# Kernel optimization log

Measured on AMD Instinct MI355X. Metric: run time of the kernel, lower is better.

The kernel has to match this reference:

```python
import jax, jax.numpy as jnp
import numpy as np

N_NODES = 100000
N_EDGES = 2000000


def setup_inputs() -> dict:
    key = jax.random.key(0)
    ks = jax.random.split(key, 8)
    x = jax.random.normal(ks[0], (N_NODES, 8), dtype=jnp.float32)
    edge_index = jax.random.randint(ks[1], (2, N_EDGES), 0, N_NODES, dtype=jnp.int64)
    W1 = jax.random.normal(ks[2], (8, 32), dtype=jnp.float32) * (1.0 / np.sqrt(8))
    b1 = jnp.zeros((32,), dtype=jnp.float32)
    W2 = jax.random.normal(ks[3], (32, 32), dtype=jnp.float32) * (1.0 / np.sqrt(32))
    b2 = jnp.zeros((32,), dtype=jnp.float32)
    Wf = jax.random.normal(ks[4], (32, 1), dtype=jnp.float32) * (1.0 / np.sqrt(32))
    bf = jnp.zeros((1,), dtype=jnp.float32)
    return {"x": x, "edge_index": edge_index, "W1": W1, "b1": b1,
            "W2": W2, "b2": b2, "Wf": Wf, "bf": bf}


def _gcn_conv(x, src, dst, norm, W, b, n_nodes):
    # x: [N, Fin] -> [N, Fout]; standard PyG GCNConv with self-loops + sym norm
    h = x @ W                                   # [N, Fout]
    msg = h[src] * norm[:, None]                # gather + scale, [E+N, Fout]
    out = jax.ops.segment_sum(msg, dst, num_segments=n_nodes)  # scatter-add
    return out + b


def reference(x, edge_index, W1, b1, W2, b2, Wf, bf):
    n = x.shape[0]
    loop = jnp.arange(n, dtype=edge_index.dtype)
    src = jnp.concatenate([edge_index[0], loop])
    dst = jnp.concatenate([edge_index[1], loop])
    # symmetric normalization: deg from target indices (incl. self-loops)
    deg = jax.ops.segment_sum(jnp.ones_like(dst, dtype=x.dtype), dst, num_segments=n)
    dis = jnp.where(deg > 0, jax.lax.rsqrt(jnp.maximum(deg, 1e-12)), 0.0)
    norm = dis[src] * dis[dst]                  # [E+N]

    h = jax.nn.relu(_gcn_conv(x, src, dst, norm, W1, b1, n))
    h = jax.nn.relu(_gcn_conv(h, src, dst, norm, W2, b2, n))
    return h @ Wf + bf                          # [N, 1]
```

## Files before the change

### kernel.cpp

```cpp
#include <hip/hip_runtime.h>
#include <hip/hip_fp16.h>


#define NBLK 256
#define SHIFT 8
#define BMASK 255
#define NBUCK 512

__global__ void k_hist(const int* __restrict__ dst, int* __restrict__ part, int E) {
    __shared__ int hist[NBUCK];
    int t = threadIdx.x;
    hist[t] = 0; hist[t + 256] = 0;
    __syncthreads();
    int E4 = E >> 2;
    int chunk4 = (E4 + NBLK - 1) / NBLK;
    int b = blockIdx.x;
    int s4 = b * chunk4;
    int e4 = min(s4 + chunk4, E4);
    const int4* dst4 = (const int4*)dst;
    for (int i = s4 + t; i < e4; i += 256) {
        int4 d = dst4[i];
        atomicAdd(&hist[d.x >> SHIFT], 1);
        atomicAdd(&hist[d.y >> SHIFT], 1);
        atomicAdd(&hist[d.z >> SHIFT], 1);
        atomicAdd(&hist[d.w >> SHIFT], 1);
    }
    if (b == NBLK - 1) {
        for (int e = (E4 << 2) + t; e < E; e += 256)
            atomicAdd(&hist[dst[e] >> SHIFT], 1);
    }
    __syncthreads();
    part[(size_t)t * NBLK + b] = hist[t];
    part[(size_t)(t + 256) * NBLK + b] = hist[t + 256];
}

__global__ void k_scanA(int* __restrict__ part, int* __restrict__ btot) {
    int t = threadIdx.x;
    int b = blockIdx.x * 4 + (t >> 6);
    int lane = t & 63;
    int4* p4 = (int4*)(part + (size_t)b * NBLK);
    int4 v = p4[lane];
    int ls = v.x + v.y + v.z + v.w;
    int s = ls;
#pragma unroll
    for (int off = 1; off < 64; off <<= 1) {
        int u = __shfl_up(s, off, 64);
        if (lane >= off) s += u;
    }
    int base = s - ls;
    int4 o;
    o.x = base;
    o.y = base + v.x;
    o.z = o.y + v.y;
    o.w = o.z + v.z;
    p4[lane] = o;
    if (lane == 63) btot[b] = s;
}

__global__ void k_scanB(const int* __restrict__ btot, int* __restrict__ bbase,
                        int* __restrict__ rowptr, int n, int E) {
    __shared__ int tmp[NBUCK];
    int t = threadIdx.x;
    int v = btot[t];
    tmp[t] = v;
    __syncthreads();
    for (int off = 1; off < NBUCK; off <<= 1) {
        int add = (t >= off) ? tmp[t - off] : 0;
        __syncthreads();
        tmp[t] += add;
        __syncthreads();
    }
    bbase[t] = tmp[t] - v;
    if (t == NBUCK - 1) bbase[NBUCK] = tmp[NBUCK - 1];
    if (t == 0) rowptr[n] = E;
}

__global__ void k_binA2(const int* __restrict__ src, const int* __restrict__ dst,
                        const int* __restrict__ part, const int* __restrict__ bbase,
                        int* __restrict__ bpair, int E) {
    __shared__ int cur[NBUCK];
    int t = threadIdx.x;
    int b = blockIdx.x;
    cur[t] = part[(size_t)t * NBLK + b] + bbase[t];
    __syncthreads();
    int E4 = E >> 2;
    int chunk4 = (E4 + NBLK - 1) / NBLK;
    int s4 = b * chunk4;
    int e4 = min(s4 + chunk4, E4);
    const int4* src4 = (const int4*)src;
    const int4* dst4 = (const int4*)dst;
    for (int i = s4 + t; i < e4; i += 512) {
        int4 s = src4[i];
        int4 d = dst4[i];
        int p0 = atomicAdd(&cur[d.x >> SHIFT], 1);
        bpair[p0] = (s.x << SHIFT) | (d.x & BMASK);
        int p1 = atomicAdd(&cur[d.y >> SHIFT], 1);
        bpair[p1] = (s.y << SHIFT) | (d.y & BMASK);
        int p2 = atomicAdd(&cur[d.z >> SHIFT], 1);
        bpair[p2] = (s.z << SHIFT) | (d.z & BMASK);
        int p3 = atomicAdd(&cur[d.w >> SHIFT], 1);
        bpair[p3] = (s.w << SHIFT) | (d.w & BMASK);
    }
    if (b == NBLK - 1) {
        for (int e = (E4 << 2) + t; e < E; e += 512) {
            int sv = src[e], dv = dst[e];
            int p = atomicAdd(&cur[dv >> SHIFT], 1);
            bpair[p] = (sv << SHIFT) | (dv & BMASK);
        }
    }
}

__global__ void k_fill2(const int* __restrict__ bpair, const int* __restrict__ bbase,
                        const float* __restrict__ x,
                        int* __restrict__ rowptr, float* __restrict__ dis,
                        unsigned int* __restrict__ xs16, int* __restrict__ col, int n) {
    __shared__ int cnt[256];
    __shared__ int tmp[256];
    __shared__ int cur[256];
    __shared__ float sdis[256];
    int b = blockIdx.x;
    int t = threadIdx.x;
    int start = bbase[b], end = bbase[b + 1];
    if (t < 256) cnt[t] = 0;
    __syncthreads();
    for (int i = start + t; i < end; i += 512)
        atomicAdd(&cnt[bpair[i] & BMASK], 1);
    __syncthreads();
    int v0 = (t < 256) ? cnt[t] : 0;
    if (t < 256) tmp[t] = v0;
    __syncthreads();
    for (int off = 1; off < 256; off <<= 1) {
        int add = (t < 256 && t >= off) ? tmp[t - off] : 0;
        __syncthreads();
        if (t < 256) tmp[t] += add;
        __syncthreads();
    }
    if (t < 256) {
        int v = (b << SHIFT) + t;
        if (v < n) {
            int r = start + tmp[t] - v0;
            rowptr[v] = r;
            cur[t] = r;
            float dv = rsqrtf(1.0f + (float)v0);
            dis[v] = dv;
            sdis[t] = dv;
        }
    }
    __syncthreads();
    int ubase = (b << SHIFT) * 4;
    int nu = n * 4;
    const float2* x2 = (const float2*)x;
    for (int i = t; i < 1024; i += 512) {
        int gi = ubase + i;
        if (gi < nu) {
            float d = sdis[i >> 2];
            float2 xv = x2[gi];
            __half2 h2 = __float22half2_rn(make_float2(xv.x * d, xv.y * d));
            xs16[gi] = *(unsigned int*)&h2;
        }
    }
    for (int i = start + t; i < end; i += 512) {
        int p = bpair[i];
        int pos = atomicAdd(&cur[p & BMASK], 1);
        col[pos] = p >> SHIFT;
    }
}

__global__ void k_g1b(const int* __restrict__ rowptr, const int* __restrict__ col,
                      const uint4* __restrict__ xs16u4, const float* __restrict__ dis,
                      const float* __restrict__ W1, const float* __restrict__ b1,
                      const float* __restrict__ W2, uint2* __restrict__ g16u2, int n) {
    __shared__ float sW1[256];
    __shared__ float sW2[1024];
    __shared__ float sh[4][8][36];
    int t = threadIdx.x;
    sW1[t] = W1[t];
    for (int i = t; i < 1024; i += 256) sW2[i] = W2[i];
    __syncthreads();
    int widx = t >> 6, lane = t & 63;
    int nd = lane >> 3, j = lane & 7;
    int v = (blockIdx.x * 4 + widx) * 8 + nd;
    float a0 = 0.f, a1 = 0.f, a2 = 0.f, a3 = 0.f,
          a4 = 0.f, a5 = 0.f, a6 = 0.f, a7 = 0.f;
    int r0 = 0, r1 = 0;
    if (v < n) { r0 = rowptr[v]; r1 = rowptr[v + 1]; }
    for (int i = r0 + j; i < r1; i += 8) {
        uint4 raw = xs16u4[col[i]];
        float2 f0 = __half22float2(*(const __half2*)&raw.x);
        float2 f1 = __half22float2(*(const __half2*)&raw.y);
        float2 f2 = __half22float2(*(const __half2*)&raw.z);
        float2 f3 = __half22float2(*(const __half2*)&raw.w);
        a0 += f0.x; a1 += f0.y; a2 += f1.x; a3 += f1.y;
        a4 += f2.x; a5 += f2.y; a6 += f3.x; a7 += f3.y;
    }
    if (j == 0 && v < n) {
        uint4 raw = xs16u4[v];
        float2 f0 = __half22float2(*(const __half2*)&raw.x);
        float2 f1 = __half22float2(*(const __half2*)&raw.y);
        float2 f2 = __half22float2(*(const __half2*)&raw.z);
        float2 f3 = __half22float2(*(const __half2*)&raw.w);
        a0 += f0.x; a1 += f0.y; a2 += f1.x; a3 += f1.y;
        a4 += f2.x; a5 += f2.y; a6 += f3.x; a7 += f3.y;
    }
#pragma unroll
    for (int m = 1; m < 8; m <<= 1) {
        a0 += __shfl_xor(a0, m, 64);
        a1 += __shfl_xor(a1, m, 64);
        a2 += __shfl_xor(a2, m, 64);
        a3 += __shfl_xor(a3, m, 64);
        a4 += __shfl_xor(a4, m, 64);
        a5 += __shfl_xor(a5, m, 64);
        a6 += __shfl_xor(a6, m, 64);
        a7 += __shfl_xor(a7, m, 64);
    }
    float dv = (v < n) ? dis[v] : 0.f;
    int f0i = j * 4;
    float h0 = 0.f, h1 = 0.f, h2 = 0.f, h3 = 0.f;
    {
        float ak[8] = {a0, a1, a2, a3, a4, a5, a6, a7};
#pragma unroll
        for (int k = 0; k < 8; ++k) {
            float4 w = *(const float4*)&sW1[k * 32 + f0i];
            h0 += ak[k] * w.x; h1 += ak[k] * w.y;
            h2 += ak[k] * w.z; h3 += ak[k] * w.w;
        }
    }
    h0 = fmaxf(dv * h0 + b1[f0i + 0], 0.f);
    h1 = fmaxf(dv * h1 + b1[f0i + 1], 0.f);
    h2 = fmaxf(dv * h2 + b1[f0i + 2], 0.f);
    h3 = fmaxf(dv * h3 + b1[f0i + 3], 0.f);
    *(float4*)&sh[widx][nd][f0i] = make_float4(h0, h1, h2, h3);
    const float4* hrow = (const float4*)&sh[widx][nd][0];
    float4 hr[8];
#pragma unroll
    for (int k4 = 0; k4 < 8; ++k4) hr[k4] = hrow[k4];
    float g0 = 0.f, g1 = 0.f, g2 = 0.f, g3 = 0.f;
#pragma unroll
    for (int k4 = 0; k4 < 8; ++k4) {
        float hk[4] = {hr[k4].x, hr[k4].y, hr[k4].z, hr[k4].w};
#pragma unroll
        for (int m = 0; m < 4; ++m) {
            float4 w = *(const float4*)&sW2[(k4 * 4 + m) * 32 + f0i];
            g0 += hk[m] * w.x; g1 += hk[m] * w.y;
            g2 += hk[m] * w.z; g3 += hk[m] * w.w;
        }
    }
    if (v < n) {
        __half2 ha = __float22half2_rn(make_float2(g0 * dv, g1 * dv));
        __half2 hb = __float22half2_rn(make_float2(g2 * dv, g3 * dv));
        uint2 o;
        o.x = *(unsigned int*)&ha;
        o.y = *(unsigned int*)&hb;
        g16u2[(size_t)v * 8 + j] = o;
    }
}

__global__ void k_g2f(const int* __restrict__ rowptr, const int* __restrict__ col,
                      const uint4* __restrict__ g16u4, const float* __restrict__ dis,
                      const float* __restrict__ b2, const float* __restrict__ Wf,
                      const float* __restrict__ bf, float* __restrict__ out, int n) {
    int t = threadIdx.x;
    int wave = t >> 6, lane = t & 63;
    int nd = lane >> 3, sub = lane & 7;
    int slot = sub >> 2, q = sub & 3;
    int v = (blockIdx.x * 4 + wave) * 8 + nd;
    if (v >= n) return;
    int r0 = rowptr[v], r1 = rowptr[v + 1];
    float4 s0 = make_float4(0.f, 0.f, 0.f, 0.f);
    float4 s1 = make_float4(0.f, 0.f, 0.f, 0.f);
    float4 t0 = make_float4(0.f, 0.f, 0.f, 0.f);
    float4 t1 = make_float4(0.f, 0.f, 0.f, 0.f);
    if (slot == 0) {
        uint4 raw = g16u4[(size_t)v * 4 + q];
        float2 f0 = __half22float2(*(const __half2*)&raw.x);
        float2 f1 = __half22float2(*(const __half2*)&raw.y);
        float2 f2 = __half22float2(*(const __half2*)&raw.z);
        float2 f3 = __half22float2(*(const __half2*)&raw.w);
        s0.x += f0.x; s0.y += f0.y; s0.z += f1.x; s0.w += f1.y;
        s1.x += f2.x; s1.y += f2.y; s1.z += f3.x; s1.w += f3.y;
    }
    int i = r0 + slot;
    for (; i + 2 < r1; i += 4) {
        int cA = col[i], cB = col[i + 2];
        uint4 rawA = g16u4[(size_t)cA * 4 + q];
        uint4 rawB = g16u4[(size_t)cB * 4 + q];
        float2 a0 = __half22float2(*(const __half2*)&rawA.x);
        float2 a1 = __half22float2(*(const __half2*)&rawA.y);
        float2 a2 = __half22float2(*(const __half2*)&rawA.z);
        float2 a3 = __half22float2(*(const __half2*)&rawA.w);
        s0.x += a0.x; s0.y += a0.y; s0.z += a1.x; s0.w += a1.y;
        s1.x += a2.x; s1.y += a2.y; s1.z += a3.x; s1.w += a3.y;
        float2 b0 = __half22float2(*(const __half2*)&rawB.x);
        float2 b1v = __half22float2(*(const __half2*)&rawB.y);
        float2 b2v = __half22float2(*(const __half2*)&rawB.z);
        float2 b3 = __half22float2(*(const __half2*)&rawB.w);
        t0.x += b0.x; t0.y += b0.y; t0.z += b1v.x; t0.w += b1v.y;
        t1.x += b2v.x; t1.y += b2v.y; t1.z += b3.x; t1.w += b3.y;
    }
    if (i < r1) {
        uint4 raw = g16u4[(size_t)col[i] * 4 + q];
        float2 f0 = __half22float2(*(const __half2*)&raw.x);
        float2 f1 = __half22float2(*(const __half2*)&raw.y);
        float2 f2 = __half22float2(*(const __half2*)&raw.z);
        float2 f3 = __half22float2(*(const __half2*)&raw.w);
        s0.x += f0.x; s0.y += f0.y; s0.z += f1.x; s0.w += f1.y;
        s1.x += f2.x; s1.y += f2.y; s1.z += f3.x; s1.w += f3.y;
    }
    s0.x += t0.x; s0.y += t0.y; s0.z += t0.z; s0.w += t0.w;
    s1.x += t1.x; s1.y += t1.y; s1.z += t1.z; s1.w += t1.w;
    s0.x += __shfl_xor(s0.x, 4, 64);
    s0.y += __shfl_xor(s0.y, 4, 64);
    s0.z += __shfl_xor(s0.z, 4, 64);
    s0.w += __shfl_xor(s0.w, 4, 64);
    s1.x += __shfl_xor(s1.x, 4, 64);
    s1.y += __shfl_xor(s1.y, 4, 64);
    s1.z += __shfl_xor(s1.z, 4, 64);
    s1.w += __shfl_xor(s1.w, 4, 64);
    float dv = dis[v];
    float4 bv0 = ((const float4*)b2)[q * 2], bv1 = ((const float4*)b2)[q * 2 + 1];
    float4 wv0 = ((const float4*)Wf)[q * 2], wv1 = ((const float4*)Wf)[q * 2 + 1];
    float p = fmaxf(dv * s0.x + bv0.x, 0.f) * wv0.x
            + fmaxf(dv * s0.y + bv0.y, 0.f) * wv0.y
            + fmaxf(dv * s0.z + bv0.z, 0.f) * wv0.z
            + fmaxf(dv * s0.w + bv0.w, 0.f) * wv0.w
            + fmaxf(dv * s1.x + bv1.x, 0.f) * wv1.x
            + fmaxf(dv * s1.y + bv1.y, 0.f) * wv1.y
            + fmaxf(dv * s1.z + bv1.z, 0.f) * wv1.z
            + fmaxf(dv * s1.w + bv1.w, 0.f) * wv1.w;
    p += __shfl_xor(p, 1, 64);
    p += __shfl_xor(p, 2, 64);
    if (sub == 0) out[v] = p + bf[0];
}

extern "C" void kernel_launch(void* const* d_in, const int* in_sizes, int n_in,
                              void* d_out, int out_size, void* d_ws, size_t ws_size,
                              hipStream_t stream) {
    const float* x  = (const float*)d_in[0];
    const int*   ei = (const int*)d_in[1];
    const float* W1 = (const float*)d_in[2];
    const float* b1 = (const float*)d_in[3];
    const float* W2 = (const float*)d_in[4];
    const float* b2 = (const float*)d_in[5];
    const float* Wf = (const float*)d_in[6];
    const float* bf = (const float*)d_in[7];
    float* out = (float*)d_out;

    const int n = in_sizes[0] / 8;
    const int E = in_sizes[1] / 2;
    const int* src = ei;
    const int* dst = ei + E;
    const int nbuck = (n + 255) >> 8;
    const size_t na = (size_t)((n + 3) & ~3);

    float* dis         = (float*)d_ws;
    unsigned int* xs16 = (unsigned int*)(dis + na);
    unsigned int* g16  = xs16 + na * 4;
    int* rowptr        = (int*)(g16 + na * 16);
    int* bbase         = rowptr + (n + 1);
    int* btot          = bbase + (NBUCK + 1);
    int* part          = btot + NBUCK + 2;
    int* col           = part + (size_t)NBUCK * NBLK;
    int* bpair         = col + E;

    k_hist <<<dim3(NBLK),      dim3(256), 0, stream>>>(dst, part, E);
    k_scanA<<<dim3(NBUCK / 4), dim3(256), 0, stream>>>(part, btot);
    k_scanB<<<dim3(1),         dim3(NBUCK), 0, stream>>>(btot, bbase, rowptr, n, E);
    k_binA2<<<dim3(NBLK),      dim3(512), 0, stream>>>(src, dst, part, bbase, bpair, E);
    k_fill2<<<dim3(nbuck),     dim3(512), 0, stream>>>(bpair, bbase, x, rowptr, dis, xs16, col, n);

    k_g1b<<<dim3((n + 31) / 32), dim3(256), 0, stream>>>(rowptr, col, (const uint4*)xs16,
                                                         dis, W1, b1, W2, (uint2*)g16, n);

    k_g2f<<<dim3((n + 31) / 32), dim3(256), 0, stream>>>(rowptr, col, (const uint4*)g16, dis,
                                                         b2, Wf, bf, out, n);
}
```

Baseline: 91.49 us.

## Split layer-2 gather into two feature-half passes for cache locality

Layer-1 output features are written as two separate half-width arrays (features 0-15 and 16-31). The layer-2 aggregation then runs twice, once per half, so each pass gathers from a smaller table that fits better in cache. Each lane now handles 4 edge slots per node instead of 2. The cost is an extra kernel launch, rereading rowptr and col twice, and a partial-sum buffer written by the first pass and combined in the second.

```diff
diff --git a/kernel.cpp b/kernel.cpp
--- a/kernel.cpp
+++ b/kernel.cpp
@@ -169,7 +169,8 @@
 __global__ void k_g1b(const int* __restrict__ rowptr, const int* __restrict__ col,
                       const uint4* __restrict__ xs16u4, const float* __restrict__ dis,
                       const float* __restrict__ W1, const float* __restrict__ b1,
-                      const float* __restrict__ W2, uint2* __restrict__ g16u2, int n) {
+                      const float* __restrict__ W2, uint2* __restrict__ g16a,
+                      uint2* __restrict__ g16b, int n) {
     __shared__ float sW1[256];
     __shared__ float sW2[1024];
     __shared__ float sh[4][8][36];
@@ -251,18 +252,20 @@
         uint2 o;
         o.x = *(unsigned int*)&ha;
         o.y = *(unsigned int*)&hb;
-        g16u2[(size_t)v * 8 + j] = o;
-    }
-}
-
-__global__ void k_g2f(const int* __restrict__ rowptr, const int* __restrict__ col,
-                      const uint4* __restrict__ g16u4, const float* __restrict__ dis,
-                      const float* __restrict__ b2, const float* __restrict__ Wf,
-                      const float* __restrict__ bf, float* __restrict__ out, int n) {
+        if (j < 4) g16a[(size_t)v * 4 + j] = o;
+        else       g16b[(size_t)v * 4 + (j - 4)] = o;
+    }
+}
+
+__global__ void k_g2h(const int* __restrict__ rowptr, const int* __restrict__ col,
+                      const uint4* __restrict__ gh, const float* __restrict__ dis,
+                      const float* __restrict__ b2o, const float* __restrict__ Wfo,
+                      const float* __restrict__ bf, float* __restrict__ partial,
+                      float* __restrict__ out, int pass, int n) {
     int t = threadIdx.x;
     int wave = t >> 6, lane = t & 63;
     int nd = lane >> 3, sub = lane & 7;
-    int slot = sub >> 2, q = sub & 3;
+    int q = sub & 1, slot = sub >> 1;
     int v = (blockIdx.x * 4 + wave) * 8 + nd;
     if (v >= n) return;
     int r0 = rowptr[v], r1 = rowptr[v + 1];
@@ -271,7 +274,7 @@
     float4 t0 = make_float4(0.f, 0.f, 0.f, 0.f);
     float4 t1 = make_float4(0.f, 0.f, 0.f, 0.f);
     if (slot == 0) {
-        uint4 raw = g16u4[(size_t)v * 4 + q];
+        uint4 raw = gh[(size_t)v * 2 + q];
         float2 f0 = __half22float2(*(const __half2*)&raw.x);
         float2 f1 = __half22float2(*(const __half2*)&raw.y);
         float2 f2 = __half22float2(*(const __half2*)&raw.z);
@@ -280,10 +283,10 @@
         s1.x += f2.x; s1.y += f2.y; s1.z += f3.x; s1.w += f3.y;
     }
     int i = r0 + slot;
-    for (; i + 2 < r1; i += 4) {
-        int cA = col[i], cB = col[i + 2];
-        uint4 rawA = g16u4[(size_t)cA * 4 + q];
-        uint4 rawB = g16u4[(size_t)cB * 4 + q];
+    for (; i + 4 < r1; i += 8) {
+        int cA = col[i], cB = col[i + 4];
+        uint4 rawA = gh[(size_t)cA * 2 + q];
+        uint4 rawB = gh[(size_t)cB * 2 + q];
         float2 a0 = __half22float2(*(const __half2*)&rawA.x);
         float2 a1 = __half22float2(*(const __half2*)&rawA.y);
         float2 a2 = __half22float2(*(const __half2*)&rawA.z);
@@ -298,7 +301,7 @@
         t1.x += b2v.x; t1.y += b2v.y; t1.z += b3.x; t1.w += b3.y;
     }
     if (i < r1) {
-        uint4 raw = g16u4[(size_t)col[i] * 4 + q];
+        uint4 raw = gh[(size_t)col[i] * 2 + q];
         float2 f0 = __half22float2(*(const __half2*)&raw.x);
         float2 f1 = __half22float2(*(const __half2*)&raw.y);
         float2 f2 = __half22float2(*(const __half2*)&raw.z);
@@ -308,17 +311,20 @@
     }
     s0.x += t0.x; s0.y += t0.y; s0.z += t0.z; s0.w += t0.w;
     s1.x += t1.x; s1.y += t1.y; s1.z += t1.z; s1.w += t1.w;
-    s0.x += __shfl_xor(s0.x, 4, 64);
-    s0.y += __shfl_xor(s0.y, 4, 64);
-    s0.z += __shfl_xor(s0.z, 4, 64);
-    s0.w += __shfl_xor(s0.w, 4, 64);
-    s1.x += __shfl_xor(s1.x, 4, 64);
-    s1.y += __shfl_xor(s1.y, 4, 64);
-    s1.z += __shfl_xor(s1.z, 4, 64);
-    s1.w += __shfl_xor(s1.w, 4, 64);
+#pragma unroll
+    for (int m = 2; m <= 4; m <<= 1) {
+        s0.x += __shfl_xor(s0.x, m, 64);
+        s0.y += __shfl_xor(s0.y, m, 64);
+        s0.z += __shfl_xor(s0.z, m, 64);
+        s0.w += __shfl_xor(s0.w, m, 64);
+        s1.x += __shfl_xor(s1.x, m, 64);
+        s1.y += __shfl_xor(s1.y, m, 64);
+        s1.z += __shfl_xor(s1.z, m, 64);
+        s1.w += __shfl_xor(s1.w, m, 64);
+    }
     float dv = dis[v];
-    float4 bv0 = ((const float4*)b2)[q * 2], bv1 = ((const float4*)b2)[q * 2 + 1];
-    float4 wv0 = ((const float4*)Wf)[q * 2], wv1 = ((const float4*)Wf)[q * 2 + 1];
+    float4 bv0 = ((const float4*)b2o)[q * 2], bv1 = ((const float4*)b2o)[q * 2 + 1];
+    float4 wv0 = ((const float4*)Wfo)[q * 2], wv1 = ((const float4*)Wfo)[q * 2 + 1];
     float p = fmaxf(dv * s0.x + bv0.x, 0.f) * wv0.x
             + fmaxf(dv * s0.y + bv0.y, 0.f) * wv0.y
             + fmaxf(dv * s0.z + bv0.z, 0.f) * wv0.z
@@ -328,8 +334,10 @@
             + fmaxf(dv * s1.z + bv1.z, 0.f) * wv1.z
             + fmaxf(dv * s1.w + bv1.w, 0.f) * wv1.w;
     p += __shfl_xor(p, 1, 64);
-    p += __shfl_xor(p, 2, 64);
-    if (sub == 0) out[v] = p + bf[0];
+    if (sub == 0) {
+        if (pass == 0) partial[v] = p;
+        else           out[v] = partial[v] + p + bf[0];
+    }
 }
 
 extern "C" void kernel_launch(void* const* d_in, const int* in_sizes, int n_in,
@@ -354,8 +362,10 @@
 
     float* dis         = (float*)d_ws;
     unsigned int* xs16 = (unsigned int*)(dis + na);
-    unsigned int* g16  = xs16 + na * 4;
-    int* rowptr        = (int*)(g16 + na * 16);
+    unsigned int* g16a = xs16 + na * 4;
+    unsigned int* g16b = g16a + na * 8;
+    float* partial     = (float*)(g16b + na * 8);
+    int* rowptr        = (int*)(partial + na);
     int* bbase         = rowptr + (n + 1);
     int* btot          = bbase + (NBUCK + 1);
     int* part          = btot + NBUCK + 2;
@@ -369,8 +379,12 @@
     k_fill2<<<dim3(nbuck),     dim3(512), 0, stream>>>(bpair, bbase, x, rowptr, dis, xs16, col, n);
 
     k_g1b<<<dim3((n + 31) / 32), dim3(256), 0, stream>>>(rowptr, col, (const uint4*)xs16,
-                                                         dis, W1, b1, W2, (uint2*)g16, n);
-
-    k_g2f<<<dim3((n + 31) / 32), dim3(256), 0, stream>>>(rowptr, col, (const uint4*)g16, dis,
-                                                         b2, Wf, bf, out, n);
-}
+                                                         dis, W1, b1, W2,
+                                                         (uint2*)g16a, (uint2*)g16b, n);
+
+    dim3 g2grid((n + 31) / 32), g2blk(256);
+    k_g2h<<<g2grid, g2blk, 0, stream>>>(rowptr, col, (const uint4*)g16a, dis,
+                                        b2, Wf, bf, partial, out, 0, n);
+    k_g2h<<<g2grid, g2blk, 0, stream>>>(rowptr, col, (const uint4*)g16b, dis,
+                                        b2 + 16, Wf + 16, bf, partial, out, 1, n);
+}
```

Result: slower. 99.10 us (+8.3%).
